# Performance work log

Measured on AMD Instinct MI355X. Metric: run time of the kernel, lower is better.

The kernel has to match this reference:

```python
import jax, jax.numpy as jnp
import numpy as np


def setup_inputs() -> dict:
    key = jax.random.key(0)
    ks = jax.random.split(key, 6)
    B, M, H = 256, 64, 512
    memory_state = jax.random.normal(ks[0], (B, M, M, M), dtype=jnp.float32) * 0.02
    hidden_state = jax.random.normal(ks[1], (B, H), dtype=jnp.float32)
    role1 = jnp.tanh(jax.random.normal(ks[2], (B, M), dtype=jnp.float32))
    role2 = jnp.tanh(jax.random.normal(ks[3], (B, M), dtype=jnp.float32))
    filer = jnp.tanh(jax.random.normal(ks[4], (B, M), dtype=jnp.float32))
    W_gate = jax.random.normal(ks[5], (1, H), dtype=jnp.float32) * (1.0 / np.sqrt(H))
    b_gate = jnp.zeros((1,), dtype=jnp.float32)
    return {"memory_state": memory_state, "hidden_state": hidden_state,
            "role1": role1, "role2": role2, "filer": filer,
            "W_gate": W_gate, "b_gate": b_gate}


def reference(memory_state, hidden_state, role1, role2, filer, W_gate, b_gate):
    M = memory_state.shape[1]
    # write gate: sigmoid(Linear(h) + 1), shape [B, 1]
    write_gate = jax.nn.sigmoid(hidden_state @ W_gate.T + b_gate + 1.0)
    # outer product of roles: [B, M, M]
    role = jnp.einsum('br,bt->brt', role1, role2)
    # read from 3D associative memory: [B, M]
    prev_info = jnp.einsum('brt,brtf->bf', role, memory_state)
    cur_info = write_gate * (filer - prev_info)
    scale = 1.0 / M
    # gated outer-product write
    new_memory = memory_state + jnp.einsum('brt,bf->brtf', role, cur_info * scale)
    # norm-clip rescale
    mem_norm = jnp.linalg.norm(new_memory.reshape(new_memory.shape[0], -1), axis=-1)
    mem_norm = jax.nn.relu(mem_norm - 1.0) + 1.0
    new_memory = new_memory / mem_norm[:, None, None, None]
    return new_memory
```

## Files before the change

### kernel.cpp

```cpp
#include <hip/hip_runtime.h>
#include <math.h>

#define M 64

typedef float f32x4 __attribute__((ext_vector_type(4)));

__device__ __forceinline__ float wave_sum64(float v) {
    #pragma unroll
    for (int m = 32; m >= 1; m >>= 1) v += __shfl_xor(v, m);
    return v;
}

__device__ __forceinline__ void reduce_part(
    const float* __restrict__ mem, const float* __restrict__ role1,
    const float* __restrict__ role2, float* __restrict__ prev_part,
    float* __restrict__ ss_part, int b, int sp)
{
    __shared__ float  role_r[512];
    __shared__ float4 part[4][16];
    __shared__ float  ss_lds[4];
    const int tid = threadIdx.x;

    for (int i = tid; i < 512; i += 256) {
        const int rt = sp * 512 + i;
        role_r[i] = role1[b * M + (rt >> 6)] * role2[b * M + (rt & 63)];
    }
    __syncthreads();

    const float4* mem4 = (const float4*)(mem + (size_t)b * 262144);
    const int f4 = tid & 15, rsub = tid >> 4;

    float4 ap = make_float4(0.f, 0.f, 0.f, 0.f);
    float  ss = 0.f;
    #pragma unroll 8
    for (int i = 0; i < 32; ++i) {
        const int lrt = rsub + i * 16;
        const float4 v = mem4[(size_t)(sp * 512 + lrt) * 16 + f4];
        const float  r = role_r[lrt];
        ap.x = fmaf(r, v.x, ap.x);
        ap.y = fmaf(r, v.y, ap.y);
        ap.z = fmaf(r, v.z, ap.z);
        ap.w = fmaf(r, v.w, ap.w);
        ss = fmaf(v.x, v.x, ss);
        ss = fmaf(v.y, v.y, ss);
        ss = fmaf(v.z, v.z, ss);
        ss = fmaf(v.w, v.w, ss);
    }

    #pragma unroll
    for (int m = 16; m <= 32; m <<= 1) {
        ap.x += __shfl_xor(ap.x, m);
        ap.y += __shfl_xor(ap.y, m);
        ap.z += __shfl_xor(ap.z, m);
        ap.w += __shfl_xor(ap.w, m);
    }
    const float ssw = wave_sum64(ss);

    const int wave = tid >> 6, lane = tid & 63;
    if (lane < 16) part[wave][lane] = ap;
    if (lane == 0) ss_lds[wave] = ssw;
    __syncthreads();

    if (tid < 16) {
        float4 a0 = part[0][tid], a1 = part[1][tid], a2 = part[2][tid], a3 = part[3][tid];
        float4 s;
        s.x = (a0.x + a1.x) + (a2.x + a3.x);
        s.y = (a0.y + a1.y) + (a2.y + a3.y);
        s.z = (a0.z + a1.z) + (a2.z + a3.z);
        s.w = (a0.w + a1.w) + (a2.w + a3.w);
        ((float4*)prev_part)[(size_t)(b * 8 + sp) * 16 + tid] = s;
    }
    if (tid == 0)
        ss_part[b * 8 + sp] = (ss_lds[0] + ss_lds[1]) + (ss_lds[2] + ss_lds[3]);
}

__device__ __forceinline__ void write_part(
    const float* __restrict__ mem, const float* __restrict__ hidden,
    const float* __restrict__ role1, const float* __restrict__ role2,
    const float* __restrict__ filer, const float* __restrict__ W_gate,
    const float* __restrict__ b_gate, const float* __restrict__ prev_part,
    const float* __restrict__ ss_part, float* __restrict__ out, int b, int ck)
{
    __shared__ float role_w[512];
    __shared__ float c2_s[M];
    __shared__ float inv_s;
    const int tid = threadIdx.x;

    if (tid < M) {
        const int f = tid;
        float p = 0.f;
        #pragma unroll
        for (int s = 0; s < 8; ++s) p += prev_part[(size_t)(b * 8 + s) * M + f];
        float ssm = 0.f;
        #pragma unroll
        for (int s = 0; s < 8; ++s) ssm += ss_part[b * 8 + s];

        float g = 0.f;
        #pragma unroll
        for (int j = 0; j < 8; ++j)
            g = fmaf(hidden[(size_t)b * 512 + f + j * 64], W_gate[f + j * 64], g);
        g = wave_sum64(g);
        g = 1.f / (1.f + expf(-(g + b_gate[0] + 1.f)));

        const float fil = filer[b * M + f];
        const float cur = g * (fil - p);
        const float d1   = wave_sum64(p * cur);
        const float ssc  = wave_sum64(cur * cur);
        const float r1   = role1[b * M + f];
        const float r2   = role2[b * M + f];
        const float ssr1 = wave_sum64(r1 * r1);
        const float ssr2 = wave_sum64(r2 * r2);

        const float sc = 1.0f / (float)M;
        const float ns = ssm + 2.f * sc * d1 + sc * sc * ssr1 * ssr2 * ssc;
        const float inv = 1.0f / fmaxf(sqrtf(ns), 1.0f);
        c2_s[f] = cur * sc * inv;
        if (f == 0) inv_s = inv;
    }
    for (int i = tid; i < 512; i += 256) {
        const int rt = ck * 512 + i;
        role_w[i] = role1[b * M + (rt >> 6)] * role2[b * M + (rt & 63)];
    }
    __syncthreads();

    const float  inv = inv_s;
    const float4 c   = ((const float4*)c2_s)[tid & 15];
    const float4* mem4 = (const float4*)(mem + (size_t)b * 262144);
    f32x4* out4 = (f32x4*)(out + (size_t)b * 262144);
    const int f4 = tid & 15, rsub = tid >> 4;

    #pragma unroll 8
    for (int i = 0; i < 32; ++i) {
        const int lrt = rsub + i * 16;
        const int idx = (ck * 512 + lrt) * 16 + f4;
        const float4 v = mem4[idx];
        const float  r = role_w[lrt];
        f32x4 o;
        o.x = fmaf(r, c.x, v.x * inv);
        o.y = fmaf(r, c.y, v.y * inv);
        o.z = fmaf(r, c.z, v.z * inv);
        o.w = fmaf(r, c.w, v.w * inv);
        __builtin_nontemporal_store(o, &out4[idx]);
    }
}

__global__ __launch_bounds__(256) void kA(
    const float* __restrict__ mem, const float* __restrict__ role1,
    const float* __restrict__ role2, float* __restrict__ prev_part,
    float* __restrict__ ss_part)
{
    reduce_part(mem, role1, role2, prev_part, ss_part,
                blockIdx.x >> 3, blockIdx.x & 7);
}

__global__ __launch_bounds__(256) void kB(
    const float* __restrict__ mem, const float* __restrict__ hidden,
    const float* __restrict__ role1, const float* __restrict__ role2,
    const float* __restrict__ filer, const float* __restrict__ W_gate,
    const float* __restrict__ b_gate, float* __restrict__ prev_part,
    float* __restrict__ ss_part, float* __restrict__ out)
{
    const int sub = blockIdx.x >> 1;
    if (blockIdx.x & 1)
        write_part(mem, hidden, role1, role2, filer, W_gate, b_gate,
                   prev_part, ss_part, out, sub >> 3, sub & 7);
    else
        reduce_part(mem, role1, role2, prev_part, ss_part,
                    128 + (sub >> 3), sub & 7);
}

__global__ __launch_bounds__(256) void kC(
    const float* __restrict__ mem, const float* __restrict__ hidden,
    const float* __restrict__ role1, const float* __restrict__ role2,
    const float* __restrict__ filer, const float* __restrict__ W_gate,
    const float* __restrict__ b_gate, const float* __restrict__ prev_part,
    const float* __restrict__ ss_part, float* __restrict__ out)
{
    write_part(mem, hidden, role1, role2, filer, W_gate, b_gate,
               prev_part, ss_part, out, 128 + (blockIdx.x >> 3), blockIdx.x & 7);
}

extern "C" void kernel_launch(void* const* d_in, const int* in_sizes, int n_in,
                              void* d_out, int out_size, void* d_ws, size_t ws_size,
                              hipStream_t stream) {
    const float* mem    = (const float*)d_in[0];
    const float* hidden = (const float*)d_in[1];
    const float* role1  = (const float*)d_in[2];
    const float* role2  = (const float*)d_in[3];
    const float* filer  = (const float*)d_in[4];
    const float* Wg     = (const float*)d_in[5];
    const float* bg     = (const float*)d_in[6];
    float* out = (float*)d_out;

    float* ws        = (float*)d_ws;
    float* prev_part = ws;
    float* ss_part   = ws + 131072;

    hipLaunchKernelGGL(kA, dim3(1024), dim3(256), 0, stream,
                       mem, role1, role2, prev_part, ss_part);
    hipLaunchKernelGGL(kB, dim3(2048), dim3(256), 0, stream,
                       mem, hidden, role1, role2, filer, Wg, bg,
                       prev_part, ss_part, out);
    hipLaunchKernelGGL(kC, dim3(1024), dim3(256), 0, stream,
                       mem, hidden, role1, role2, filer, Wg, bg,
                       prev_part, ss_part, out);
}
```

Baseline: 144.3 us.

## Replace three-kernel staggered overlap with plain reduce-then-write two-kernel schedule

Removes the interleaved schedule in which the middle kernel ran write blocks for the first half of the batch alongside reduce blocks for the second half. It now launches one reduce kernel over all 256 batches, then one write kernel over all batches. This simplifies the code and drops one launch, but gives up the overlap of the read-heavy reduce phase with the write-heavy phase. Index math also drops the size_t cast in the reduce load.

```diff
diff --git a/kernel.cpp b/kernel.cpp
--- a/kernel.cpp
+++ b/kernel.cpp
@@ -2,6 +2,8 @@
 #include <math.h>
 
 #define M 64
+#define B 256
+#define T 256
 
 typedef float f32x4 __attribute__((ext_vector_type(4)));
 
@@ -11,19 +13,22 @@
     return v;
 }
 
-__device__ __forceinline__ void reduce_part(
+__global__ __launch_bounds__(T) void k_reduce(
     const float* __restrict__ mem, const float* __restrict__ role1,
     const float* __restrict__ role2, float* __restrict__ prev_part,
-    float* __restrict__ ss_part, int b, int sp)
+    float* __restrict__ ss_part)
 {
-    __shared__ float  role_r[512];
+    const int b   = blockIdx.x >> 3;
+    const int sp  = blockIdx.x & 7;
+    const int tid = threadIdx.x;
+
+    __shared__ float  role_s[512];
     __shared__ float4 part[4][16];
     __shared__ float  ss_lds[4];
-    const int tid = threadIdx.x;
 
-    for (int i = tid; i < 512; i += 256) {
+    for (int i = tid; i < 512; i += T) {
         const int rt = sp * 512 + i;
-        role_r[i] = role1[b * M + (rt >> 6)] * role2[b * M + (rt & 63)];
+        role_s[i] = role1[b * M + (rt >> 6)] * role2[b * M + (rt & 63)];
     }
     __syncthreads();
 
@@ -35,8 +40,8 @@
     #pragma unroll 8
     for (int i = 0; i < 32; ++i) {
         const int lrt = rsub + i * 16;
-        const float4 v = mem4[(size_t)(sp * 512 + lrt) * 16 + f4];
-        const float  r = role_r[lrt];
+        const float4 v = mem4[(sp * 512 + lrt) * 16 + f4];
+        const float  r = role_s[lrt];
         ap.x = fmaf(r, v.x, ap.x);
         ap.y = fmaf(r, v.y, ap.y);
         ap.z = fmaf(r, v.z, ap.z);
@@ -74,17 +79,20 @@
         ss_part[b * 8 + sp] = (ss_lds[0] + ss_lds[1]) + (ss_lds[2] + ss_lds[3]);
 }
 
-__device__ __forceinline__ void write_part(
+__global__ __launch_bounds__(T) void k_write(
     const float* __restrict__ mem, const float* __restrict__ hidden,
     const float* __restrict__ role1, const float* __restrict__ role2,
     const float* __restrict__ filer, const float* __restrict__ W_gate,
     const float* __restrict__ b_gate, const float* __restrict__ prev_part,
-    const float* __restrict__ ss_part, float* __restrict__ out, int b, int ck)
+    const float* __restrict__ ss_part, float* __restrict__ out)
 {
-    __shared__ float role_w[512];
+    const int b   = blockIdx.x >> 3;
+    const int sp  = blockIdx.x & 7;
+    const int tid = threadIdx.x;
+
+    __shared__ float role_s[512];
     __shared__ float c2_s[M];
     __shared__ float inv_s;
-    const int tid = threadIdx.x;
 
     if (tid < M) {
         const int f = tid;
@@ -117,9 +125,9 @@
         c2_s[f] = cur * sc * inv;
         if (f == 0) inv_s = inv;
     }
-    for (int i = tid; i < 512; i += 256) {
-        const int rt = ck * 512 + i;
-        role_w[i] = role1[b * M + (rt >> 6)] * role2[b * M + (rt & 63)];
+    for (int i = tid; i < 512; i += T) {
+        const int rt = sp * 512 + i;
+        role_s[i] = role1[b * M + (rt >> 6)] * role2[b * M + (rt & 63)];
     }
     __syncthreads();
 
@@ -132,9 +140,9 @@
     #pragma unroll 8
     for (int i = 0; i < 32; ++i) {
         const int lrt = rsub + i * 16;
-        const int idx = (ck * 512 + lrt) * 16 + f4;
+        const int idx = (sp * 512 + lrt) * 16 + f4;
         const float4 v = mem4[idx];
-        const float  r = role_w[lrt];
+        const float  r = role_s[lrt];
         f32x4 o;
         o.x = fmaf(r, c.x, v.x * inv);
         o.y = fmaf(r, c.y, v.y * inv);
@@ -142,42 +150,6 @@
         o.w = fmaf(r, c.w, v.w * inv);
         __builtin_nontemporal_store(o, &out4[idx]);
     }
-}
-
-__global__ __launch_bounds__(256) void kA(
-    const float* __restrict__ mem, const float* __restrict__ role1,
-    const float* __restrict__ role2, float* __restrict__ prev_part,
-    float* __restrict__ ss_part)
-{
-    reduce_part(mem, role1, role2, prev_part, ss_part,
-                blockIdx.x >> 3, blockIdx.x & 7);
-}
-
-__global__ __launch_bounds__(256) void kB(
-    const float* __restrict__ mem, const float* __restrict__ hidden,
-    const float* __restrict__ role1, const float* __restrict__ role2,
-    const float* __restrict__ filer, const float* __restrict__ W_gate,
-    const float* __restrict__ b_gate, float* __restrict__ prev_part,
-    float* __restrict__ ss_part, float* __restrict__ out)
-{
-    const int sub = blockIdx.x >> 1;
-    if (blockIdx.x & 1)
-        write_part(mem, hidden, role1, role2, filer, W_gate, b_gate,
-                   prev_part, ss_part, out, sub >> 3, sub & 7);
-    else
-        reduce_part(mem, role1, role2, prev_part, ss_part,
-                    128 + (sub >> 3), sub & 7);
-}
-
-__global__ __launch_bounds__(256) void kC(
-    const float* __restrict__ mem, const float* __restrict__ hidden,
-    const float* __restrict__ role1, const float* __restrict__ role2,
-    const float* __restrict__ filer, const float* __restrict__ W_gate,
-    const float* __restrict__ b_gate, const float* __restrict__ prev_part,
-    const float* __restrict__ ss_part, float* __restrict__ out)
-{
-    write_part(mem, hidden, role1, role2, filer, W_gate, b_gate,
-               prev_part, ss_part, out, 128 + (blockIdx.x >> 3), blockIdx.x & 7);
 }
 
 extern "C" void kernel_launch(void* const* d_in, const int* in_sizes, int n_in,
@@ -196,12 +168,9 @@
     float* prev_part = ws;
     float* ss_part   = ws + 131072;
 
-    hipLaunchKernelGGL(kA, dim3(1024), dim3(256), 0, stream,
+    hipLaunchKernelGGL(k_reduce, dim3(B * 8), dim3(T), 0, stream,
                        mem, role1, role2, prev_part, ss_part);
-    hipLaunchKernelGGL(kB, dim3(2048), dim3(256), 0, stream,
-                       mem, hidden, role1, role2, filer, Wg, bg,
-                       prev_part, ss_part, out);
-    hipLaunchKernelGGL(kC, dim3(1024), dim3(256), 0, stream,
+    hipLaunchKernelGGL(k_write, dim3(B * 8), dim3(T), 0, stream,
                        mem, hidden, role1, role2, filer, Wg, bg,
                        prev_part, ss_part, out);
 }
```

After: 131.4 us, median of 2. 9.0% less time.
